# Performance work log

Measured on AMD Instinct MI355X. Metric: run time of the kernel, lower is better.

## Reference

```python
import jax, jax.numpy as jnp
import numpy as np

B, S, D_MODEL, N_HEADS = 4, 2048, 2048, 16
HEAD_DIM = D_MODEL // N_HEADS  # 128
ROT_HALF = HEAD_DIM // 2       # 64


def _make_rope(max_pos, half_dim, base=10000.0):
    inv_freq = 1.0 / (base ** (np.arange(0, half_dim, dtype=np.float32) / half_dim))
    t = np.arange(max_pos, dtype=np.float32)
    freqs = np.outer(t, inv_freq)  # (max_pos, half_dim)
    return jnp.asarray(np.cos(freqs)), jnp.asarray(np.sin(freqs))


def setup_inputs() -> dict:
    key = jax.random.key(0)
    k1, k2, k3 = jax.random.split(key, 3)
    x = jax.random.normal(k1, (B, S, D_MODEL), dtype=jnp.float32)
    w_qkv = jax.random.normal(k2, (D_MODEL, 3 * D_MODEL), dtype=jnp.float32) * (D_MODEL ** -0.5)
    b_qkv = jnp.zeros((3 * D_MODEL,), dtype=jnp.float32)
    w_out = jax.random.normal(k3, (D_MODEL, D_MODEL), dtype=jnp.float32) * (D_MODEL ** -0.5)
    b_out = jnp.zeros((D_MODEL,), dtype=jnp.float32)
    rotary_cos, rotary_sin = _make_rope(S, ROT_HALF)
    return {"x": x, "w_qkv": w_qkv, "b_qkv": b_qkv, "w_out": w_out,
            "b_out": b_out, "rotary_cos": rotary_cos, "rotary_sin": rotary_sin}


def _apply_rope(q, k, cos, sin):
    # q, k: (B, H, S, Dh); cos, sin: (S, Dh//2)
    cos = cos[None, None, :, :]
    sin = sin[None, None, :, :]

    def _rotate(t):
        even = t[..., 0::2]
        odd = t[..., 1::2]
        r_even = even * cos - odd * sin
        r_odd = even * sin + odd * cos
        return jnp.stack([r_even, r_odd], axis=-1).reshape(t.shape)

    return _rotate(q), _rotate(k)


def reference(x, w_qkv, b_qkv, w_out, b_out, rotary_cos, rotary_sin):
    batch, seq, _ = x.shape
    scale = HEAD_DIM ** -0.5
    # Fused QKV projection, split into heads
    qkv = x @ w_qkv + b_qkv                                   # (B, S, 3*D)
    qkv = qkv.reshape(batch, seq, 3, N_HEADS, HEAD_DIM)
    qkv = jnp.transpose(qkv, (2, 0, 3, 1, 4))                 # (3, B, H, S, Dh)
    q, k, v = qkv[0], qkv[1], qkv[2]
    # RoPE at pos_offset = 0
    q, k = _apply_rope(q, k, rotary_cos[:seq], rotary_sin[:seq])
    # Causal scaled dot-product attention
    scores = jnp.einsum("bhqd,bhkd->bhqk", q, k) * scale      # (B, H, S, S)
    causal = jnp.tril(jnp.ones((seq, seq), dtype=bool))
    scores = jnp.where(causal, scores, jnp.finfo(scores.dtype).min)
    attn = jax.nn.softmax(scores, axis=-1)
    out = jnp.einsum("bhqk,bhkd->bhqd", attn, v)              # (B, H, S, Dh)
    out = jnp.transpose(out, (0, 2, 1, 3)).reshape(batch, seq, D_MODEL)
    return out @ w_out + b_out
```

## Files before the change

### kernel.cpp

```cpp
#include <hip/hip_runtime.h>
#include <stdint.h>

#define B_  4
#define S_  2048
#define DM_ 2048
#define NH_ 16
#define HD_ 128

typedef unsigned short u16;
typedef unsigned int   u32;
typedef __attribute__((ext_vector_type(8))) short short8;
typedef __attribute__((ext_vector_type(8))) unsigned short u16x8;
typedef __attribute__((ext_vector_type(4))) float f32x4;
typedef __attribute__((ext_vector_type(16))) float f32x16;

__device__ __forceinline__ u16 f2b(float f){
  union { float f; unsigned u; } v; v.f = f;
  return (u16)((v.u + 0x7fffu + ((v.u >> 16) & 1u)) >> 16);
}
__device__ __forceinline__ float b2f(u16 b){
  union { unsigned u; float f; } v; v.u = ((unsigned)b) << 16; return v.f;
}
__device__ __forceinline__ void gld_lds16(const void* g, void* l){
  __builtin_amdgcn_global_load_lds(
    (const __attribute__((address_space(1))) unsigned int*)(uintptr_t)g,
    (__attribute__((address_space(3))) unsigned int*)(uintptr_t)l, 16, 0, 0);
}

__global__ void k_convert(const float* __restrict__ in, u16* __restrict__ out, int n){
  int i = (blockIdx.x * 256 + threadIdx.x) * 8;
  if (i >= n) return;
  float4 a = *(const float4*)(in + i);
  float4 b = *(const float4*)(in + i + 4);
  u16x8 o;
  o[0]=f2b(a.x); o[1]=f2b(a.y); o[2]=f2b(a.z); o[3]=f2b(a.w);
  o[4]=f2b(b.x); o[5]=f2b(b.y); o[6]=f2b(b.z); o[7]=f2b(b.w);
  *(u16x8*)(out + i) = o;
}

__global__ void k_transpose_cvt(const float* __restrict__ in, u16* __restrict__ out,
                                int R, int C){
  __shared__ u16 tile[32][33];
  int tx = threadIdx.x, ty = threadIdx.y;
  int c0 = blockIdx.x * 32, r0 = blockIdx.y * 32;
  #pragma unroll
  for (int i = 0; i < 4; i++){
    int r = r0 + ty + i * 8;
    tile[ty + i*8][tx] = f2b(in[(size_t)r * C + c0 + tx]);
  }
  __syncthreads();
  #pragma unroll
  for (int i = 0; i < 4; i++){
    int c = c0 + ty + i * 8;
    out[(size_t)c * R + r0 + tx] = tile[tx][ty + i*8];
  }
}

template<int EPI>
__global__ __launch_bounds__(256, 2) void k_gemm_bt(
    const u16* __restrict__ A, const u16* __restrict__ BT,
    const float* __restrict__ bias,
    u16* __restrict__ Qd, u16* __restrict__ Kd, u16* __restrict__ Vd,
    float* __restrict__ Cout)
{
  __shared__ u16 As[128 * 32];
  __shared__ u16 Bs[128 * 32];
  const int lane = threadIdx.x & 63;
  const int wid  = threadIdx.x >> 6;
  const int wr = wid >> 1, wc = wid & 1;
  const int m0 = blockIdx.x * 128;
  const int n0 = blockIdx.y * 128;
  f32x4 acc[4][4] = {};
  const int fr = lane & 15;
  const int ks = (lane >> 4) * 8;

  for (int k0 = 0; k0 < 2048; k0 += 32){
    __syncthreads();
    #pragma unroll
    for (int t = 0; t < 2; t++){
      const int ob  = wid * 2048 + t * 1024 + lane * 16;
      const int row = ob >> 6, colb = ob & 63;
      gld_lds16(A  + (size_t)(m0 + row) * 2048 + k0 + (colb >> 1),
                (char*)As + wid * 2048 + t * 1024);
      gld_lds16(BT + (size_t)(n0 + row) * 2048 + k0 + (colb >> 1),
                (char*)Bs + wid * 2048 + t * 1024);
    }
    __syncthreads();
    short8 af[4], bf[4];
    #pragma unroll
    for (int i = 0; i < 4; i++) af[i] = *(const short8*)&As[(wr*64 + i*16 + fr)*32 + ks];
    #pragma unroll
    for (int i = 0; i < 4; i++) bf[i] = *(const short8*)&Bs[(wc*64 + i*16 + fr)*32 + ks];
    #pragma unroll
    for (int i = 0; i < 4; i++)
      #pragma unroll
      for (int j = 0; j < 4; j++)
        acc[i][j] = __builtin_amdgcn_mfma_f32_16x16x32_bf16(af[i], bf[j], acc[i][j], 0, 0, 0);
  }

  const int rowb = m0 + wr*64 + (lane >> 4) * 4;
  const int colb = n0 + wc*64 + (lane & 15);
  #pragma unroll
  for (int ni = 0; ni < 4; ni++){
    const int col = colb + ni * 16;
    const float bv = bias[col];
    if (EPI == 0){
      const int qkv = col >> 11, hd = col & 2047, h = hd >> 7, d = hd & 127;
      u16* dst = (qkv == 0) ? Qd : ((qkv == 1) ? Kd : Vd);
      #pragma unroll
      for (int mi = 0; mi < 4; mi++){
        f32x4 c = acc[mi][ni];
        #pragma unroll
        for (int j = 0; j < 4; j++){
          const int row = rowb + mi * 16 + j;
          const int b = row >> 11, s = row & 2047;
          size_t idx;
          if (qkv == 2) idx = ((size_t)((b * NH_ + h) * HD_ + d)) * S_ + s;
          else          idx = ((size_t)((b * NH_ + h) * S_  + s)) * HD_ + d;
          dst[idx] = f2b(c[j] + bv);
        }
      }
    } else {
      #pragma unroll
      for (int mi = 0; mi < 4; mi++){
        f32x4 c = acc[mi][ni];
        #pragma unroll
        for (int j = 0; j < 4; j++){
          const int row = rowb + mi * 16 + j;
          Cout[(size_t)row * 2048 + col] = c[j] + bv;
        }
      }
    }
  }
}

__global__ void k_rope(u16* __restrict__ Qb, u16* __restrict__ Kb,
                       const float* __restrict__ rc, const float* __restrict__ rs){
  const int gid = blockIdx.x * 256 + threadIdx.x;
  const int seg = gid & 3;
  const int row = gid >> 2;
  const int NR  = B_ * NH_ * S_;
  u16* base = (row < NR) ? (Qb + (size_t)row * HD_) : (Kb + (size_t)(row - NR) * HD_);
  const int s  = row & (S_ - 1);
  const int d0 = seg * 32;
  u16x8 v[4];
  #pragma unroll
  for (int t = 0; t < 4; t++) v[t] = *(u16x8*)(base + d0 + t * 8);
  float c[16], sn[16];
  const float4* cp = (const float4*)(rc + (size_t)s * 64 + seg * 16);
  const float4* sp = (const float4*)(rs + (size_t)s * 64 + seg * 16);
  #pragma unroll
  for (int t = 0; t < 4; t++){
    float4 cv = cp[t], sv = sp[t];
    c[t*4+0]=cv.x; c[t*4+1]=cv.y; c[t*4+2]=cv.z; c[t*4+3]=cv.w;
    sn[t*4+0]=sv.x; sn[t*4+1]=sv.y; sn[t*4+2]=sv.z; sn[t*4+3]=sv.w;
  }
  #pragma unroll
  for (int p = 0; p < 16; p++){
    int t = p >> 2, l = (2 * p) & 7;
    float e = b2f(v[t][l]), o = b2f(v[t][l + 1]);
    v[t][l]     = f2b(e * c[p] - o * sn[p]);
    v[t][l + 1] = f2b(e * sn[p] + o * c[p]);
  }
  #pragma unroll
  for (int t = 0; t < 4; t++) *(u16x8*)(base + d0 + t * 8) = v[t];
}

#define KVB 64
__global__ __launch_bounds__(256, 2) void k_attn(
    const u16* __restrict__ Qb, const u16* __restrict__ Kb,
    const u16* __restrict__ Vtb, u16* __restrict__ Ob)
{
  const int bh = blockIdx.y;
  const int qt = (int)gridDim.x - 1 - (int)blockIdx.x;
  const int lane = threadIdx.x & 63, wid = threadIdx.x >> 6;
  const int q = lane & 31, hi = lane >> 5;
  const int b = bh >> 4, h = bh & 15;
  const u16* Qp = Qb  + (size_t)bh * S_ * HD_;
  const u16* Kp = Kb  + (size_t)bh * S_ * HD_;
  const u16* Vp = Vtb + (size_t)bh * HD_ * S_;
  __shared__ u16 Ks[KVB * HD_];
  __shared__ u16 Vs[HD_ * KVB];

  const int q0w  = qt * 128 + wid * 32;
  const int q_abs = q0w + q;

  short8 qf[8];
  {
    const u16* qrow = Qp + (size_t)q_abs * HD_ + hi * 8;
    #pragma unroll
    for (int s = 0; s < 8; s++) qf[s] = *(const short8*)(qrow + s * 16);
  }
  f32x16 oacc[4] = {};
  float mrun = -__builtin_inff(), lrun = 0.f;
  const float scale = 0.08838834764831845f;
  const int nt = 2 * qt + 2;
  const int base16 = wid * 256 + lane;

  for (int it = 0; it < nt; ++it){
    const int kv0 = it * KVB;
    __syncthreads();
    #pragma unroll
    for (int c = 0; c < 4; c++){
      const int idx = base16 + c * 64;
      const int r  = idx >> 4, y  = idx & 15;
      const int r2 = idx >> 3, y2 = idx & 7;
      gld_lds16(Kp + (size_t)(kv0 + r) * HD_ + ((y ^ (r & 15)) << 3),
                (char*)Ks + ((wid * 256 + c * 64) << 4));
      gld_lds16(Vp + (size_t)r2 * S_ + kv0 + ((y2 ^ (r2 & 7)) << 3),
                (char*)Vs + ((wid * 256 + c * 64) << 4));
    }
    __syncthreads();
    if (kv0 > q0w + 31) continue;

    f32x16 sacc[2] = {};
    #pragma unroll
    for (int s = 0; s < 8; s++)
      #pragma unroll
      for (int kb = 0; kb < 2; kb++){
        const int row  = kb * 32 + q;
        const int slot = (2 * s + hi) ^ (q & 15);
        short8 kf = *(const short8*)((const char*)Ks + row * 256 + slot * 16);
        sacc[kb] = __builtin_amdgcn_mfma_f32_32x32x16_bf16(kf, qf[s], sacc[kb], 0, 0, 0);
      }

    float pmax = -__builtin_inff();
    #pragma unroll
    for (int kb = 0; kb < 2; kb++)
      #pragma unroll
      for (int i = 0; i < 16; i++){
        const int k_abs = kv0 + kb * 32 + (i & 3) + 8 * (i >> 2) + 4 * hi;
        const float sv = (k_abs <= q_abs) ? sacc[kb][i] * scale : -__builtin_inff();
        sacc[kb][i] = sv;
        pmax = fmaxf(pmax, sv);
      }
    pmax = fmaxf(pmax, __shfl_xor(pmax, 32));
    const float mnew = fmaxf(mrun, pmax);
    const float sc = __expf(mrun - mnew);
    float rsum = 0.f;
    #pragma unroll
    for (int kb = 0; kb < 2; kb++)
      #pragma unroll
      for (int i = 0; i < 16; i++){
        const float e = __expf(sacc[kb][i] - mnew);
        sacc[kb][i] = e; rsum += e;
      }
    rsum += __shfl_xor(rsum, 32);
    lrun = lrun * sc + rsum; mrun = mnew;

    #pragma unroll
    for (int i = 0; i < 16; i++){
      const float s_i = __shfl(sc, (i & 3) + 8 * (i >> 2) + 4 * hi);
      #pragma unroll
      for (int n4 = 0; n4 < 4; n4++) oacc[n4][i] *= s_i;
    }

    u32 wds[2][8];
    #pragma unroll
    for (int kb = 0; kb < 2; kb++)
      #pragma unroll
      for (int t = 0; t < 8; t++)
        wds[kb][t] = (u32)f2b(sacc[kb][2*t]) | ((u32)f2b(sacc[kb][2*t+1]) << 16);

    #pragma unroll
    for (int sp = 0; sp < 4; sp++){
      const int kb = sp >> 1, hh = sp & 1;
      const u32 w0 = wds[kb][4*hh+0], w1 = wds[kb][4*hh+1];
      const u32 w2 = wds[kb][4*hh+2], w3 = wds[kb][4*hh+3];
      const int x0 = __shfl((int)w0, q + 32);
      const int x1 = __shfl((int)w1, q + 32);
      const int y0 = __shfl((int)w2, q);
      const int y1 = __shfl((int)w3, q);
      union { int w[4]; short8 v; } pa;
      pa.w[0] = hi ? y0 : (int)w0;
      pa.w[1] = hi ? y1 : (int)w1;
      pa.w[2] = hi ? (int)w2 : x0;
      pa.w[3] = hi ? (int)w3 : x1;
      #pragma unroll
      for (int n4 = 0; n4 < 4; n4++){
        const int d = n4 * 32 + q;
        const int slot = (2 * sp + hi) ^ (d & 7);
        short8 vf = *(const short8*)((const char*)Vs + d * 128 + slot * 16);
        oacc[n4] = __builtin_amdgcn_mfma_f32_32x32x16_bf16(pa.v, vf, oacc[n4], 0, 0, 0);
      }
    }
  }

  const float inv = 1.0f / lrun;
  #pragma unroll
  for (int i = 0; i < 16; i++){
    const int r = (i & 3) + 8 * (i >> 2) + 4 * hi;
    const float linv = __shfl(inv, r);
    const int row = q0w + r;
    u16* orow = Ob + ((size_t)(b * S_ + row) * DM_) + h * HD_ + q;
    #pragma unroll
    for (int n4 = 0; n4 < 4; n4++)
      orow[n4 * 32] = f2b(oacc[n4][i] * linv);
  }
}

extern "C" void kernel_launch(void* const* d_in, const int* in_sizes, int n_in,
                              void* d_out, int out_size, void* d_ws, size_t ws_size,
                              hipStream_t stream) {
  const float* x     = (const float*)d_in[0];
  const float* w_qkv = (const float*)d_in[1];
  const float* b_qkv = (const float*)d_in[2];
  const float* w_out = (const float*)d_in[3];
  const float* b_out = (const float*)d_in[4];
  const float* rc    = (const float*)d_in[5];
  const float* rs    = (const float*)d_in[6];
  char* ws = (char*)d_ws;
  u16* xb    = (u16*)(ws);
  u16* wqkvT = (u16*)(ws + 33554432ull);
  u16* woutT = (u16*)(ws + 58720256ull);
  u16* Qb    = (u16*)(ws + 67108864ull);
  u16* Kb    = (u16*)(ws + 100663296ull);
  u16* Vt    = (u16*)(ws + 134217728ull);
  u16* AO    = xb;
  float* out = (float*)d_out;

  k_convert<<<8192, 256, 0, stream>>>(x, xb, 16777216);
  k_transpose_cvt<<<dim3(192, 64), dim3(32, 8), 0, stream>>>(w_qkv, wqkvT, 2048, 6144);
  k_transpose_cvt<<<dim3(64, 64),  dim3(32, 8), 0, stream>>>(w_out, woutT, 2048, 2048);
  k_gemm_bt<0><<<dim3(64, 48), 256, 0, stream>>>(xb, wqkvT, b_qkv, Qb, Kb, Vt, nullptr);
  k_rope<<<4096, 256, 0, stream>>>(Qb, Kb, rc, rs);
  k_attn<<<dim3(16, 64), 256, 0, stream>>>(Qb, Kb, Vt, AO);
  k_gemm_bt<1><<<dim3(64, 16), 256, 0, stream>>>(AO, woutT, b_out, nullptr, nullptr, nullptr, out);
}
```

Baseline: 747.2 us.

## Rewrite projection GEMMs with 256x256 tiles, double-buffered swizzled LDS pipeline

Replaces the 128x128, single-buffered bf16 GEMM with a 512-thread kernel that computes 256x256 output tiles over K-steps of 64. It uses two LDS buffers with asynchronous global-to-LDS loads issued two stages ahead, an XOR swizzle on LDS rows to avoid bank conflicts, and an XCD-aware block index remap. MFMA blocks are interleaved with LDS reads under s_setprio to overlap compute and memory. The goal is more data reuse and less barrier and load latency in both projection GEMMs. The costs are 128KB of LDS, occupancy of one block per CU, and fewer workgroups (256 for the output GEMM), which may leave some CUs idle.

```diff
diff --git a/kernel.cpp b/kernel.cpp
--- a/kernel.cpp
+++ b/kernel.cpp
@@ -56,50 +56,120 @@
   }
 }
 
+#define NT_K 32
 template<int EPI>
-__global__ __launch_bounds__(256, 2) void k_gemm_bt(
+__global__ __launch_bounds__(512, 1) void k_gemm256(
     const u16* __restrict__ A, const u16* __restrict__ BT,
     const float* __restrict__ bias,
     u16* __restrict__ Qd, u16* __restrict__ Kd, u16* __restrict__ Vd,
     float* __restrict__ Cout)
 {
-  __shared__ u16 As[128 * 32];
-  __shared__ u16 Bs[128 * 32];
-  const int lane = threadIdx.x & 63;
-  const int wid  = threadIdx.x >> 6;
-  const int wr = wid >> 1, wc = wid & 1;
-  const int m0 = blockIdx.x * 128;
-  const int n0 = blockIdx.y * 128;
-  f32x4 acc[4][4] = {};
-  const int fr = lane & 15;
-  const int ks = (lane >> 4) * 8;
-
-  for (int k0 = 0; k0 < 2048; k0 += 32){
-    __syncthreads();
-    #pragma unroll
-    for (int t = 0; t < 2; t++){
-      const int ob  = wid * 2048 + t * 1024 + lane * 16;
-      const int row = ob >> 6, colb = ob & 63;
-      gld_lds16(A  + (size_t)(m0 + row) * 2048 + k0 + (colb >> 1),
-                (char*)As + wid * 2048 + t * 1024);
-      gld_lds16(BT + (size_t)(n0 + row) * 2048 + k0 + (colb >> 1),
-                (char*)Bs + wid * 2048 + t * 1024);
-    }
-    __syncthreads();
-    short8 af[4], bf[4];
-    #pragma unroll
-    for (int i = 0; i < 4; i++) af[i] = *(const short8*)&As[(wr*64 + i*16 + fr)*32 + ks];
-    #pragma unroll
-    for (int i = 0; i < 4; i++) bf[i] = *(const short8*)&Bs[(wc*64 + i*16 + fr)*32 + ks];
-    #pragma unroll
-    for (int i = 0; i < 4; i++)
-      #pragma unroll
-      for (int j = 0; j < 4; j++)
-        acc[i][j] = __builtin_amdgcn_mfma_f32_16x16x32_bf16(af[i], bf[j], acc[i][j], 0, 0, 0);
-  }
-
-  const int rowb = m0 + wr*64 + (lane >> 4) * 4;
-  const int colb = n0 + wc*64 + (lane & 15);
+  __shared__ u16 As[2][256 * 64];
+  __shared__ u16 Bs[2][256 * 64];
+  const int tid  = threadIdx.x;
+  const int lane = tid & 63, wid = tid >> 6;
+  const int wr = wid >> 2, wc = wid & 3;
+  const int fr = lane & 15, g = lane >> 4;
+
+  const int nwg = (int)gridDim.x;
+  const int cpx = nwg >> 3;
+  const int swz = ((int)blockIdx.x & 7) * cpx + ((int)blockIdx.x >> 3);
+  const int m0 = (swz & 31) * 256;
+  const int n0 = (swz >> 5) * 256;
+
+  f32x4 acc[8][4] = {};
+
+  auto STAGE = [&](int buf, int kt){
+    const int k0 = kt * 64;
+    #pragma unroll
+    for (int c = 0; c < 4; c++){
+      const int Lb = wid * 1024 + c * 8192;
+      const int L  = Lb + lane * 16;
+      const int R  = L >> 7;
+      const int Cp = L & 127;
+      const int Cl = Cp ^ ((R & 7) << 4);
+      gld_lds16(A  + (size_t)(m0 + R) * 2048 + k0 + (Cl >> 1), (char*)As[buf] + Lb);
+      gld_lds16(BT + (size_t)(n0 + R) * 2048 + k0 + (Cl >> 1), (char*)Bs[buf] + Lb);
+    }
+  };
+  auto LDA = [&](int buf, int mi, int s) -> short8 {
+    const int R  = wr * 128 + mi * 16 + fr;
+    const int Cl = s * 64 + g * 16;
+    return *(const short8*)((const char*)As[buf] + R * 128 + (Cl ^ ((R & 7) << 4)));
+  };
+  auto LDB = [&](int buf, int ni, int s) -> short8 {
+    const int R  = wc * 64 + ni * 16 + fr;
+    const int Cl = s * 64 + g * 16;
+    return *(const short8*)((const char*)Bs[buf] + R * 128 + (Cl ^ ((R & 7) << 4)));
+  };
+  auto COMPUTE = [&](int buf){
+    short8 a[4][2], b[4][2];
+    #pragma unroll
+    for (int mi = 0; mi < 4; mi++){ a[mi][0] = LDA(buf, mi, 0); a[mi][1] = LDA(buf, mi, 1); }
+    #pragma unroll
+    for (int ni = 0; ni < 2; ni++){ b[ni][0] = LDB(buf, ni, 0); b[ni][1] = LDB(buf, ni, 1); }
+    __builtin_amdgcn_s_setprio(1);
+    #pragma unroll
+    for (int mi = 0; mi < 4; mi++)
+      #pragma unroll
+      for (int ni = 0; ni < 2; ni++)
+        #pragma unroll
+        for (int s = 0; s < 2; s++)
+          acc[mi][ni] = __builtin_amdgcn_mfma_f32_16x16x32_bf16(a[mi][s], b[ni][s], acc[mi][ni], 0, 0, 0);
+    __builtin_amdgcn_s_setprio(0);
+    #pragma unroll
+    for (int ni = 2; ni < 4; ni++){ b[ni][0] = LDB(buf, ni, 0); b[ni][1] = LDB(buf, ni, 1); }
+    __builtin_amdgcn_s_setprio(1);
+    #pragma unroll
+    for (int mi = 0; mi < 4; mi++)
+      #pragma unroll
+      for (int ni = 2; ni < 4; ni++)
+        #pragma unroll
+        for (int s = 0; s < 2; s++)
+          acc[mi][ni] = __builtin_amdgcn_mfma_f32_16x16x32_bf16(a[mi][s], b[ni][s], acc[mi][ni], 0, 0, 0);
+    __builtin_amdgcn_s_setprio(0);
+    #pragma unroll
+    for (int mi = 0; mi < 4; mi++){ a[mi][0] = LDA(buf, mi + 4, 0); a[mi][1] = LDA(buf, mi + 4, 1); }
+    __builtin_amdgcn_s_setprio(1);
+    #pragma unroll
+    for (int mi = 0; mi < 4; mi++)
+      #pragma unroll
+      for (int ni = 2; ni < 4; ni++)
+        #pragma unroll
+        for (int s = 0; s < 2; s++)
+          acc[mi+4][ni] = __builtin_amdgcn_mfma_f32_16x16x32_bf16(a[mi][s], b[ni][s], acc[mi+4][ni], 0, 0, 0);
+    __builtin_amdgcn_s_setprio(0);
+    __builtin_amdgcn_s_setprio(1);
+    #pragma unroll
+    for (int mi = 0; mi < 4; mi++)
+      #pragma unroll
+      for (int ni = 0; ni < 2; ni++)
+        #pragma unroll
+        for (int s = 0; s < 2; s++)
+          acc[mi+4][ni] = __builtin_amdgcn_mfma_f32_16x16x32_bf16(a[mi][s], b[ni][s], acc[mi+4][ni], 0, 0, 0);
+    __builtin_amdgcn_s_setprio(0);
+  };
+
+  STAGE(0, 0);
+  STAGE(1, 1);
+  for (int t = 0; t < NT_K - 1; ++t){
+    const int cur = t & 1;
+    asm volatile("s_waitcnt vmcnt(8)" ::: "memory");
+    __builtin_amdgcn_s_barrier();
+    __builtin_amdgcn_sched_barrier(0);
+    COMPUTE(cur);
+    __builtin_amdgcn_sched_barrier(0);
+    __builtin_amdgcn_s_barrier();
+    __builtin_amdgcn_sched_barrier(0);
+    if (t + 2 < NT_K) STAGE(cur, t + 2);
+  }
+  asm volatile("s_waitcnt vmcnt(0)" ::: "memory");
+  __builtin_amdgcn_s_barrier();
+  __builtin_amdgcn_sched_barrier(0);
+  COMPUTE((NT_K - 1) & 1);
+
+  const int rowb = m0 + wr * 128 + g * 4;
+  const int colb = n0 + wc * 64 + fr;
   #pragma unroll
   for (int ni = 0; ni < 4; ni++){
     const int col = colb + ni * 16;
@@ -108,7 +178,7 @@
       const int qkv = col >> 11, hd = col & 2047, h = hd >> 7, d = hd & 127;
       u16* dst = (qkv == 0) ? Qd : ((qkv == 1) ? Kd : Vd);
       #pragma unroll
-      for (int mi = 0; mi < 4; mi++){
+      for (int mi = 0; mi < 8; mi++){
         f32x4 c = acc[mi][ni];
         #pragma unroll
         for (int j = 0; j < 4; j++){
@@ -122,7 +192,7 @@
       }
     } else {
       #pragma unroll
-      for (int mi = 0; mi < 4; mi++){
+      for (int mi = 0; mi < 8; mi++){
         f32x4 c = acc[mi][ni];
         #pragma unroll
         for (int j = 0; j < 4; j++){
@@ -322,8 +392,8 @@
   k_convert<<<8192, 256, 0, stream>>>(x, xb, 16777216);
   k_transpose_cvt<<<dim3(192, 64), dim3(32, 8), 0, stream>>>(w_qkv, wqkvT, 2048, 6144);
   k_transpose_cvt<<<dim3(64, 64),  dim3(32, 8), 0, stream>>>(w_out, woutT, 2048, 2048);
-  k_gemm_bt<0><<<dim3(64, 48), 256, 0, stream>>>(xb, wqkvT, b_qkv, Qb, Kb, Vt, nullptr);
+  k_gemm256<0><<<768, 512, 0, stream>>>(xb, wqkvT, b_qkv, Qb, Kb, Vt, nullptr);
   k_rope<<<4096, 256, 0, stream>>>(Qb, Kb, rc, rs);
   k_attn<<<dim3(16, 64), 256, 0, stream>>>(Qb, Kb, Vt, AO);
-  k_gemm_bt<1><<<dim3(64, 16), 256, 0, stream>>>(AO, woutT, b_out, nullptr, nullptr, nullptr, out);
-}
+  k_gemm256<1><<<256, 512, 0, stream>>>(AO, woutT, b_out, nullptr, nullptr, nullptr, out);
+}
```

Result: faster. 731.2 us (-2.1%).
